# Performance work log

Measured on AMD Instinct MI355X. Metric: run time of the kernel, lower is better.

The kernel has to match this reference:

```python
import jax, jax.numpy as jnp
import numpy as np

EPS = 1e-7
N_NODES = 100000

# --- Lorentz model (c = 1), working at the origin o = (1, 0, ..., 0) ---

def expmap0(v_spatial):
    """Exp map at origin: tangent spatial part [N, d] -> hyperboloid point [N, d+1]."""
    nrm = jnp.sqrt(jnp.maximum(jnp.sum(v_spatial * v_spatial, axis=-1, keepdims=True), EPS))
    x0 = jnp.cosh(nrm)
    xs = jnp.sinh(nrm) / nrm * v_spatial
    return jnp.concatenate([x0, xs], axis=-1)


def logmap0(x):
    """Log map at origin: point [N, d+1] -> tangent spatial part [N, d]."""
    x0 = jnp.maximum(x[..., :1], 1.0 + EPS)
    xs = x[..., 1:]
    nrm = jnp.sqrt(jnp.maximum(jnp.sum(xs * xs, axis=-1, keepdims=True), EPS))
    return jnp.arccosh(x0) / nrm * xs


def sigmoid_nonlin(x):
    # log map -> sigmoid in tangent space -> exp map (c_in = c_out = 1)
    return expmap0(jax.nn.sigmoid(logmap0(x)))


def hgcn_layer(x, edge_index, W, b):
    """HGCN conv: tangent-space linear + mean aggregation over edges + exp map."""
    t = logmap0(x)                      # [N, d_in]
    h = t @ W + b                       # [N, d_out]
    src, dst = edge_index[0], edge_index[1]
    msg = h[src]                        # [E, d_out] gather
    agg = jax.ops.segment_sum(msg, dst, num_segments=N_NODES)
    deg = jax.ops.segment_sum(jnp.ones((edge_index.shape[1],), h.dtype), dst,
                              num_segments=N_NODES)
    agg = agg / jnp.maximum(deg, 1.0)[:, None]
    return expmap0(agg)


def setup_inputs() -> dict:
    key = jax.random.key(0)
    ks = jax.random.split(key, 10)
    d_in, h1, h2, h_mlp, d_out = 64, 64, 64, 128, 40
    return {
        "features": jax.random.normal(ks[0], (N_NODES, d_in), jnp.float32),
        "edge_index": jax.random.randint(ks[1], (2, 1600000), 0, N_NODES, jnp.int64),
        "W1": jax.random.normal(ks[2], (d_in, h1), jnp.float32) * 0.05,
        "b1": jnp.zeros((h1,), jnp.float32),
        "W2": jax.random.normal(ks[3], (h1, h2), jnp.float32) * 0.05,
        "b2": jnp.zeros((h2,), jnp.float32),
        "W3": jax.random.normal(ks[4], (h2, h_mlp), jnp.float32) * 0.05,
        "b3": jnp.zeros((h_mlp,), jnp.float32),
        "W4": jax.random.normal(ks[5], (h_mlp, d_out), jnp.float32) * 0.05,
        "b4": jnp.zeros((d_out,), jnp.float32),
    }


def reference(features, edge_index, W1, b1, W2, b2, W3, b3, W4, b4):
    # lift Euclidean features to the hyperboloid (pad time coord, exp map)
    x = expmap0(features)                       # [N, d_in+1]
    x = hgcn_layer(x, edge_index, W1, b1)
    x = sigmoid_nonlin(x)
    x = hgcn_layer(x, edge_index, W2, b2)
    x = sigmoid_nonlin(x)
    t = logmap0(x)                              # [N, h2] (spatial part, drops time coord)
    # MLP head (dropout inactive at eval)
    h = jax.nn.relu(t @ W3 + b3)
    return h @ W4 + b4
```

## Files before the change

kernel.cpp:

```cpp
#include <hip/hip_runtime.h>


constexpr int CSHIFT = 9;
constexpr int CNODES = 1 << CSHIFT;
constexpr int EPB    = 4096;
constexpr int EPT    = EPB / 256;
constexpr int CAP    = 16384;

constexpr int W1F_OFF = 0;
constexpr int W2F_OFF = 4096;
constexpr int W3F_OFF = 8192;
constexpr int W4F_OFF = 16384;
constexpr int WIMG_TOT = 22528;

typedef __attribute__((ext_vector_type(8))) short short8;
typedef __attribute__((ext_vector_type(4))) float floatx4;

__device__ __forceinline__ float sigmoidf(float x) {
    return 1.0f / (1.0f + __expf(-x));
}
__device__ __forceinline__ unsigned short f2bf(float f) {
    unsigned int u = __float_as_uint(f);
    u = (u + 0x7FFFu + ((u >> 16) & 1u)) >> 16;
    return (unsigned short)u;
}

__global__ __launch_bounds__(256) void prep_cast_k(
    const float* __restrict__ feat, unsigned short* __restrict__ featbf,
    const float* __restrict__ W1, const float* __restrict__ W2,
    const float* __restrict__ W3, const float* __restrict__ W4,
    unsigned short* __restrict__ img, int n8)
{
    int i = blockIdx.x * 256 + threadIdx.x;
    if (i < n8) {
        const float4* p = (const float4*)feat + (size_t)i * 2;
        float4 a = p[0], b = p[1];
        uint4 o;
        o.x = (unsigned)f2bf(a.x) | ((unsigned)f2bf(a.y) << 16);
        o.y = (unsigned)f2bf(a.z) | ((unsigned)f2bf(a.w) << 16);
        o.z = (unsigned)f2bf(b.x) | ((unsigned)f2bf(b.y) << 16);
        o.w = (unsigned)f2bf(b.z) | ((unsigned)f2bf(b.w) << 16);
        ((uint4*)featbf)[i] = o;
        return;
    }
    int t = i - n8;
    if (t >= WIMG_TOT) return;
    float v = 0.f;
    int s = t;
    if (s < W2F_OFF) {
        int j = s & 7, m = (s >> 3) & 15, q = (s >> 7) & 3, kk = (s >> 9) & 1, c = s >> 10;
        v = W1[(kk * 32 + q * 8 + j) * 64 + c * 16 + m];
    } else if (s < W3F_OFF) {
        s -= W2F_OFF;
        int j = s & 7, m = (s >> 3) & 15, q = (s >> 7) & 3, kk = (s >> 9) & 1, c = s >> 10;
        v = W2[(kk * 32 + q * 8 + j) * 64 + c * 16 + m];
    } else if (s < W4F_OFF) {
        s -= W3F_OFF;
        int j = s & 7, m = (s >> 3) & 15, q = (s >> 7) & 3, kk = (s >> 9) & 1, c = s >> 10;
        v = W3[(kk * 32 + q * 8 + j) * 128 + c * 16 + m];
    } else {
        s -= W4F_OFF;
        int j = s & 7, m = (s >> 3) & 15, q = (s >> 7) & 3, kk = (s >> 9) & 3, c = s >> 11;
        int n = c * 16 + m;
        if (n < 40) v = W4[(kk * 32 + q * 8 + j) * 40 + n];
    }
    img[t] = f2bf(v);
}

__global__ __launch_bounds__(256) void part_a(const int* __restrict__ src,
                                              const int* __restrict__ dst,
                                              int* __restrict__ ccur,
                                              int* __restrict__ arena,
                                              int E, int NBUCK) {
    __shared__ int  hist[256];
    __shared__ int  exoff[256];
    __shared__ int  lcur[256];
    __shared__ int  gbase[256];
    __shared__ int  stage[EPB];
    __shared__ unsigned char stageB[EPB];

    const int tid = threadIdx.x;
    const int e0  = blockIdx.x * EPB;
    const int ec  = min(EPB, E - e0);

    int pk[EPT], bk[EPT];
    hist[tid] = 0;
    __syncthreads();
    #pragma unroll
    for (int j = 0; j < EPT; j++) {
        int idx = tid + j * 256;
        if (idx < ec) {
            int s = src[e0 + idx];
            int d = dst[e0 + idx];
            bk[j] = d >> CSHIFT;
            pk[j] = s | ((d & (CNODES - 1)) << 17);
            atomicAdd(&hist[bk[j]], 1);
        } else bk[j] = -1;
    }
    __syncthreads();
    const int h = hist[tid];
    exoff[tid] = h;
    __syncthreads();
    for (int dd = 1; dd < 256; dd <<= 1) {
        int v = 0;
        if (tid >= dd) v = exoff[tid - dd];
        __syncthreads();
        if (tid >= dd) exoff[tid] += v;
        __syncthreads();
    }
    const int ex = exoff[tid] - h;
    int gb = 0;
    if (tid < NBUCK && h > 0) gb = atomicAdd(ccur + tid, h);
    __syncthreads();
    exoff[tid] = ex;
    lcur[tid]  = ex;
    gbase[tid] = gb;
    __syncthreads();
    #pragma unroll
    for (int j = 0; j < EPT; j++) {
        if (bk[j] >= 0) {
            int l = atomicAdd(&lcur[bk[j]], 1);
            stage[l]  = pk[j];
            stageB[l] = (unsigned char)bk[j];
        }
    }
    __syncthreads();
    for (int i = tid; i < ec; i += 256) {
        int b = stageB[i];
        arena[(size_t)b * CAP + gbase[b] + (i - exoff[b])] = stage[i];
    }
}

__global__ __launch_bounds__(256) void csr_fine(const int* __restrict__ arena,
                                                const int* __restrict__ ccur,
                                                int* __restrict__ off,
                                                int* __restrict__ ssrc,
                                                int N, int E, int NBUCK) {
    __shared__ int cnt[CNODES];
    __shared__ int cur[CNODES];
    __shared__ int part[256];
    const int b = blockIdx.x;
    const int node0 = b << CSHIFT;
    const int tid = threadIdx.x;

    part[tid] = (tid < NBUCK) ? ccur[tid] : 0;
    __syncthreads();
    for (int d = 1; d < 256; d <<= 1) {
        int v = 0;
        if (tid >= d) v = part[tid - d];
        __syncthreads();
        if (tid >= d) part[tid] += v;
        __syncthreads();
    }
    const int cbeg = (b > 0) ? part[b - 1] : 0;
    const int ec   = ccur[b];
    if (b == 0 && tid == 0) off[N] = E;
    __syncthreads();

    const int* pe = arena + (size_t)b * CAP;
    cnt[tid] = 0;
    cnt[tid + 256] = 0;
    __syncthreads();
    for (int i = tid; i < ec; i += 256)
        atomicAdd(&cnt[(pe[i] >> 17) & (CNODES - 1)], 1);
    __syncthreads();
    const int c0 = cnt[2 * tid], c1 = cnt[2 * tid + 1];
    part[tid] = c0 + c1;
    __syncthreads();
    for (int d = 1; d < 256; d <<= 1) {
        int v = 0;
        if (tid >= d) v = part[tid - d];
        __syncthreads();
        if (tid >= d) part[tid] += v;
        __syncthreads();
    }
    const int ex = (tid > 0) ? part[tid - 1] : 0;
    cur[2 * tid]     = ex;
    cur[2 * tid + 1] = ex + c0;
    if (node0 + 2 * tid     < N) off[node0 + 2 * tid]     = cbeg + ex;
    if (node0 + 2 * tid + 1 < N) off[node0 + 2 * tid + 1] = cbeg + ex + c0;
    __syncthreads();
    for (int i = tid; i < ec; i += 256) {
        int p = pe[i];
        int pos = cbeg + atomicAdd(&cur[(p >> 17) & (CNODES - 1)], 1);
        ssrc[pos] = p & 0x1FFFF;
    }
}

#define ACC8(v)                                    \
    acc[0] += __uint_as_float((v).x << 16);        \
    acc[1] += __uint_as_float((v).x & 0xFFFF0000u);\
    acc[2] += __uint_as_float((v).y << 16);        \
    acc[3] += __uint_as_float((v).y & 0xFFFF0000u);\
    acc[4] += __uint_as_float((v).z << 16);        \
    acc[5] += __uint_as_float((v).z & 0xFFFF0000u);\
    acc[6] += __uint_as_float((v).w << 16);        \
    acc[7] += __uint_as_float((v).w & 0xFFFF0000u);

__global__ __launch_bounds__(256) void agg_k(const unsigned short* __restrict__ h,
                                             const int* __restrict__ off,
                                             const int* __restrict__ ssrc,
                                             unsigned short* __restrict__ outb,
                                             int N) {
    int t = blockIdx.x * 256 + threadIdx.x;
    int g = t >> 3;
    if (g >= N) return;
    int q = (t & 7) * 8;
    int beg = off[g], end = off[g + 1];
    float acc[8] = {0.f, 0.f, 0.f, 0.f, 0.f, 0.f, 0.f, 0.f};
    int i = beg;
    for (; i + 8 <= end; i += 8) {
        uint4 v0 = *(const uint4*)(h + (size_t)ssrc[i]     * 64 + q);
        uint4 v1 = *(const uint4*)(h + (size_t)ssrc[i + 1] * 64 + q);
        uint4 v2 = *(const uint4*)(h + (size_t)ssrc[i + 2] * 64 + q);
        uint4 v3 = *(const uint4*)(h + (size_t)ssrc[i + 3] * 64 + q);
        uint4 v4 = *(const uint4*)(h + (size_t)ssrc[i + 4] * 64 + q);
        uint4 v5 = *(const uint4*)(h + (size_t)ssrc[i + 5] * 64 + q);
        uint4 v6 = *(const uint4*)(h + (size_t)ssrc[i + 6] * 64 + q);
        uint4 v7 = *(const uint4*)(h + (size_t)ssrc[i + 7] * 64 + q);
        ACC8(v0); ACC8(v1); ACC8(v2); ACC8(v3);
        ACC8(v4); ACC8(v5); ACC8(v6); ACC8(v7);
    }
    for (; i + 2 <= end; i += 2) {
        uint4 v0 = *(const uint4*)(h + (size_t)ssrc[i]     * 64 + q);
        uint4 v1 = *(const uint4*)(h + (size_t)ssrc[i + 1] * 64 + q);
        ACC8(v0); ACC8(v1);
    }
    for (; i < end; i++) {
        uint4 v = *(const uint4*)(h + (size_t)ssrc[i] * 64 + q);
        ACC8(v);
    }
    float inv = 1.0f / (float)max(end - beg, 1);
    uint4 p;
    p.x = (unsigned)f2bf(acc[0] * inv) | ((unsigned)f2bf(acc[1] * inv) << 16);
    p.y = (unsigned)f2bf(acc[2] * inv) | ((unsigned)f2bf(acc[3] * inv) << 16);
    p.z = (unsigned)f2bf(acc[4] * inv) | ((unsigned)f2bf(acc[5] * inv) << 16);
    p.w = (unsigned)f2bf(acc[6] * inv) | ((unsigned)f2bf(acc[7] * inv) << 16);
    *(uint4*)(outb + (size_t)g * 64 + q) = p;
}

__global__ __launch_bounds__(256) void gemmsig_k(
    const unsigned short* __restrict__ Abf, const int* __restrict__ off,
    const unsigned short* __restrict__ img, const float* __restrict__ bias,
    unsigned short* __restrict__ out, int N)
{
    const int tid = threadIdx.x;
    const int rowB = blockIdx.x * 64;
    const int w = tid >> 6, lane = tid & 63;
    const int m = lane & 15, quad = lane >> 4;
    const int row0 = rowB + w * 16;
    const int arow = min(row0 + m, N - 1);
    const short8* Wf = (const short8*)(img + W1F_OFF);

    floatx4 acc[4];
    #pragma unroll
    for (int c = 0; c < 4; c++) acc[c] = (floatx4){0.f, 0.f, 0.f, 0.f};
    #pragma unroll
    for (int kk = 0; kk < 2; kk++) {
        short8 a = *(const short8*)(Abf + (size_t)arow * 64 + kk * 32 + quad * 8);
        #pragma unroll
        for (int c = 0; c < 4; c++) {
            short8 b = Wf[((c * 2 + kk) * 4 + quad) * 16 + m];
            acc[c] = __builtin_amdgcn_mfma_f32_16x16x32_bf16(a, b, acc[c], 0, 0, 0);
        }
    }
    bool dzr[4];
    int rows[4];
    #pragma unroll
    for (int r = 0; r < 4; r++) {
        rows[r] = row0 + quad * 4 + r;
        dzr[r] = (rows[r] < N) ? (off[rows[r] + 1] == off[rows[r]]) : false;
    }
    #pragma unroll
    for (int c = 0; c < 4; c++) {
        int col = c * 16 + m;
        float bv = bias[col];
        #pragma unroll
        for (int r = 0; r < 4; r++) {
            if (rows[r] < N) {
                float v = dzr[r] ? 0.5f : sigmoidf(acc[c][r] + bv);
                out[(size_t)rows[r] * 64 + col] = f2bf(v);
            }
        }
    }
}

__global__ __launch_bounds__(256) void ep3b_k(
    const unsigned short* __restrict__ Abf, const int* __restrict__ off,
    const unsigned short* __restrict__ img,
    const float* __restrict__ b2, const float* __restrict__ b3,
    const float* __restrict__ b4, float* __restrict__ out, int N)
{
    __shared__ alignas(16) unsigned short T2[64 * 72];
    __shared__ alignas(16) unsigned short H3[64 * 136];

    const int tid = threadIdx.x;
    const int rowB = blockIdx.x * 64;
    const int w = tid >> 6, lane = tid & 63;
    const int m = lane & 15, quad = lane >> 4;
    const int row0 = rowB + w * 16;

    {
        const short8* Wf = (const short8*)(img + W2F_OFF);
        floatx4 acc[4];
        #pragma unroll
        for (int c = 0; c < 4; c++) acc[c] = (floatx4){0.f, 0.f, 0.f, 0.f};
        const int arow = min(row0 + m, N - 1);
        #pragma unroll
        for (int kk = 0; kk < 2; kk++) {
            short8 a = *(const short8*)(Abf + (size_t)arow * 64 + kk * 32 + quad * 8);
            #pragma unroll
            for (int c = 0; c < 4; c++) {
                short8 b = Wf[((c * 2 + kk) * 4 + quad) * 16 + m];
                acc[c] = __builtin_amdgcn_mfma_f32_16x16x32_bf16(a, b, acc[c], 0, 0, 0);
            }
        }
        bool dzr[4];
        #pragma unroll
        for (int r = 0; r < 4; r++) {
            int row = row0 + quad * 4 + r;
            dzr[r] = (row < N) ? (off[row + 1] == off[row]) : false;
        }
        #pragma unroll
        for (int c = 0; c < 4; c++) {
            int col = c * 16 + m;
            float bv = b2[col];
            #pragma unroll
            for (int r = 0; r < 4; r++) {
                int rl = w * 16 + quad * 4 + r;
                float v = dzr[r] ? 0.5f : sigmoidf(acc[c][r] + bv);
                T2[rl * 72 + col] = f2bf(v);
            }
        }
    }
    __syncthreads();

    {
        const short8* Wf = (const short8*)(img + W3F_OFF);
        floatx4 acc[8];
        #pragma unroll
        for (int c = 0; c < 8; c++) acc[c] = (floatx4){0.f, 0.f, 0.f, 0.f};
        #pragma unroll
        for (int kk = 0; kk < 2; kk++) {
            short8 a = *(const short8*)(T2 + (w * 16 + m) * 72 + kk * 32 + quad * 8);
            #pragma unroll
            for (int c = 0; c < 8; c++) {
                short8 b = Wf[((c * 2 + kk) * 4 + quad) * 16 + m];
                acc[c] = __builtin_amdgcn_mfma_f32_16x16x32_bf16(a, b, acc[c], 0, 0, 0);
            }
        }
        #pragma unroll
        for (int c = 0; c < 8; c++) {
            int col = c * 16 + m;
            float bv = b3[col];
            #pragma unroll
            for (int r = 0; r < 4; r++) {
                int rl = w * 16 + quad * 4 + r;
                H3[rl * 136 + col] = f2bf(fmaxf(acc[c][r] + bv, 0.f));
            }
        }
    }
    __syncthreads();

    {
        const short8* Wf = (const short8*)(img + W4F_OFF);
        floatx4 acc[3];
        #pragma unroll
        for (int c = 0; c < 3; c++) acc[c] = (floatx4){0.f, 0.f, 0.f, 0.f};
        #pragma unroll
        for (int kk = 0; kk < 4; kk++) {
            short8 a = *(const short8*)(H3 + (w * 16 + m) * 136 + kk * 32 + quad * 8);
            #pragma unroll
            for (int c = 0; c < 3; c++) {
                short8 b = Wf[((c * 4 + kk) * 4 + quad) * 16 + m];
                acc[c] = __builtin_amdgcn_mfma_f32_16x16x32_bf16(a, b, acc[c], 0, 0, 0);
            }
        }
        #pragma unroll
        for (int c = 0; c < 3; c++) {
            int col = c * 16 + m;
            if (col < 40) {
                float bv = b4[col];
                #pragma unroll
                for (int r = 0; r < 4; r++) {
                    int row = row0 + quad * 4 + r;
                    if (row < N) out[(size_t)row * 40 + col] = acc[c][r] + bv;
                }
            }
        }
    }
}

extern "C" void kernel_launch(void* const* d_in, const int* in_sizes, int n_in,
                              void* d_out, int out_size, void* d_ws, size_t ws_size,
                              hipStream_t stream)
{
    const float* feat = (const float*)d_in[0];
    const int*   eidx = (const int*)d_in[1];
    const float* W1 = (const float*)d_in[2];
    const float* b1 = (const float*)d_in[3];
    const float* W2 = (const float*)d_in[4];
    const float* b2 = (const float*)d_in[5];
    const float* W3 = (const float*)d_in[6];
    const float* b3 = (const float*)d_in[7];
    const float* W4 = (const float*)d_in[8];
    const float* b4 = (const float*)d_in[9];

    const int N = in_sizes[0] / 64;
    const int E = in_sizes[1] / 2;
    const int* src = eidx;
    const int* dst = eidx + E;

    const int NBUCK = (N + CNODES - 1) / CNODES;

    unsigned short* featbf = (unsigned short*)d_ws;
    unsigned short* t1     = featbf + (size_t)N * 64;
    unsigned short* aggF   = t1     + (size_t)N * 64;
    unsigned short* img    = aggF   + (size_t)N * 64;
    int*   off   = (int*)(img + WIMG_TOT);
    int*   ccur  = off + (N + 1);
    int*   ssrc  = ccur + NBUCK;
    int*   arena = ssrc + E;
    float* out   = (float*)d_out;

    hipMemsetAsync(ccur, 0, (size_t)NBUCK * sizeof(int), stream);

    const dim3 blk(256);
    const int gP  = (E + EPB - 1) / EPB;
    const int g64 = (N + 63) / 64;
    const int n8  = N * 64 / 8;
    const int gPC = (n8 + WIMG_TOT + 255) / 256;
    const int gAg = (int)(((size_t)N * 8 + 255) / 256);

    prep_cast_k<<<gPC, blk, 0, stream>>>(feat, featbf, W1, W2, W3, W4, img, n8);
    part_a<<<gP, blk, 0, stream>>>(src, dst, ccur, arena, E, NBUCK);
    csr_fine<<<NBUCK, blk, 0, stream>>>(arena, ccur, off, ssrc, N, E, NBUCK);

    agg_k<<<gAg, blk, 0, stream>>>(featbf, off, ssrc, aggF, N);
    gemmsig_k<<<g64, blk, 0, stream>>>(aggF, off, img, b1, t1, N);
    agg_k<<<gAg, blk, 0, stream>>>(t1, off, ssrc, aggF, N);
    ep3b_k<<<g64, blk, 0, stream>>>(aggF, off, img, b2, b3, b4, out, N);
}
```

Baseline: 235.9 us.

## Fuse neighbor aggregation into the following GEMM kernels via shared-memory tiles

Each 64-row block now gathers and mean-aggregates its rows' neighbor features into an LDS tile, then runs the MFMA GEMM straight from LDS. This removes two separate aggregation kernels and the global round trip of the aggregated buffer. In exchange, each thread handles two rows serially, so a block's gather has less parallelism and is exposed to degree imbalance. The second fused kernel shares LDS between the gather tile and H3 and adds a barrier to prevent overwriting.

```diff
diff --git a/kernel.cpp b/kernel.cpp
--- a/kernel.cpp
+++ b/kernel.cpp
@@ -197,59 +197,66 @@
     acc[6] += __uint_as_float((v).w << 16);        \
     acc[7] += __uint_as_float((v).w & 0xFFFF0000u);
 
-__global__ __launch_bounds__(256) void agg_k(const unsigned short* __restrict__ h,
-                                             const int* __restrict__ off,
-                                             const int* __restrict__ ssrc,
-                                             unsigned short* __restrict__ outb,
-                                             int N) {
-    int t = blockIdx.x * 256 + threadIdx.x;
-    int g = t >> 3;
-    if (g >= N) return;
-    int q = (t & 7) * 8;
-    int beg = off[g], end = off[g + 1];
-    float acc[8] = {0.f, 0.f, 0.f, 0.f, 0.f, 0.f, 0.f, 0.f};
-    int i = beg;
-    for (; i + 8 <= end; i += 8) {
-        uint4 v0 = *(const uint4*)(h + (size_t)ssrc[i]     * 64 + q);
-        uint4 v1 = *(const uint4*)(h + (size_t)ssrc[i + 1] * 64 + q);
-        uint4 v2 = *(const uint4*)(h + (size_t)ssrc[i + 2] * 64 + q);
-        uint4 v3 = *(const uint4*)(h + (size_t)ssrc[i + 3] * 64 + q);
-        uint4 v4 = *(const uint4*)(h + (size_t)ssrc[i + 4] * 64 + q);
-        uint4 v5 = *(const uint4*)(h + (size_t)ssrc[i + 5] * 64 + q);
-        uint4 v6 = *(const uint4*)(h + (size_t)ssrc[i + 6] * 64 + q);
-        uint4 v7 = *(const uint4*)(h + (size_t)ssrc[i + 7] * 64 + q);
-        ACC8(v0); ACC8(v1); ACC8(v2); ACC8(v3);
-        ACC8(v4); ACC8(v5); ACC8(v6); ACC8(v7);
-    }
-    for (; i + 2 <= end; i += 2) {
-        uint4 v0 = *(const uint4*)(h + (size_t)ssrc[i]     * 64 + q);
-        uint4 v1 = *(const uint4*)(h + (size_t)ssrc[i + 1] * 64 + q);
-        ACC8(v0); ACC8(v1);
-    }
-    for (; i < end; i++) {
-        uint4 v = *(const uint4*)(h + (size_t)ssrc[i] * 64 + q);
-        ACC8(v);
-    }
-    float inv = 1.0f / (float)max(end - beg, 1);
-    uint4 p;
-    p.x = (unsigned)f2bf(acc[0] * inv) | ((unsigned)f2bf(acc[1] * inv) << 16);
-    p.y = (unsigned)f2bf(acc[2] * inv) | ((unsigned)f2bf(acc[3] * inv) << 16);
-    p.z = (unsigned)f2bf(acc[4] * inv) | ((unsigned)f2bf(acc[5] * inv) << 16);
-    p.w = (unsigned)f2bf(acc[6] * inv) | ((unsigned)f2bf(acc[7] * inv) << 16);
-    *(uint4*)(outb + (size_t)g * 64 + q) = p;
-}
-
-__global__ __launch_bounds__(256) void gemmsig_k(
-    const unsigned short* __restrict__ Abf, const int* __restrict__ off,
-    const unsigned short* __restrict__ img, const float* __restrict__ bias,
-    unsigned short* __restrict__ out, int N)
+__device__ __forceinline__ void gather_tile(
+    const unsigned short* __restrict__ h, const int* __restrict__ off,
+    const int* __restrict__ ssrc, unsigned short* Agg, int rowB, int N, int tid)
 {
+    #pragma unroll
+    for (int pass = 0; pass < 2; pass++) {
+        int rl = pass * 32 + (tid >> 3);
+        int g  = rowB + rl;
+        int q  = (tid & 7) * 8;
+        uint4 p = make_uint4(0u, 0u, 0u, 0u);
+        if (g < N) {
+            int beg = off[g], end = off[g + 1];
+            float acc[8] = {0.f, 0.f, 0.f, 0.f, 0.f, 0.f, 0.f, 0.f};
+            int i = beg;
+            for (; i + 8 <= end; i += 8) {
+                uint4 v0 = *(const uint4*)(h + (size_t)ssrc[i]     * 64 + q);
+                uint4 v1 = *(const uint4*)(h + (size_t)ssrc[i + 1] * 64 + q);
+                uint4 v2 = *(const uint4*)(h + (size_t)ssrc[i + 2] * 64 + q);
+                uint4 v3 = *(const uint4*)(h + (size_t)ssrc[i + 3] * 64 + q);
+                uint4 v4 = *(const uint4*)(h + (size_t)ssrc[i + 4] * 64 + q);
+                uint4 v5 = *(const uint4*)(h + (size_t)ssrc[i + 5] * 64 + q);
+                uint4 v6 = *(const uint4*)(h + (size_t)ssrc[i + 6] * 64 + q);
+                uint4 v7 = *(const uint4*)(h + (size_t)ssrc[i + 7] * 64 + q);
+                ACC8(v0); ACC8(v1); ACC8(v2); ACC8(v3);
+                ACC8(v4); ACC8(v5); ACC8(v6); ACC8(v7);
+            }
+            for (; i + 2 <= end; i += 2) {
+                uint4 v0 = *(const uint4*)(h + (size_t)ssrc[i]     * 64 + q);
+                uint4 v1 = *(const uint4*)(h + (size_t)ssrc[i + 1] * 64 + q);
+                ACC8(v0); ACC8(v1);
+            }
+            for (; i < end; i++) {
+                uint4 v = *(const uint4*)(h + (size_t)ssrc[i] * 64 + q);
+                ACC8(v);
+            }
+            float inv = 1.0f / (float)max(end - beg, 1);
+            p.x = (unsigned)f2bf(acc[0]*inv) | ((unsigned)f2bf(acc[1]*inv) << 16);
+            p.y = (unsigned)f2bf(acc[2]*inv) | ((unsigned)f2bf(acc[3]*inv) << 16);
+            p.z = (unsigned)f2bf(acc[4]*inv) | ((unsigned)f2bf(acc[5]*inv) << 16);
+            p.w = (unsigned)f2bf(acc[6]*inv) | ((unsigned)f2bf(acc[7]*inv) << 16);
+        }
+        *(uint4*)(Agg + rl * 72 + q) = p;
+    }
+}
+
+__global__ __launch_bounds__(256) void aggemm1_k(
+    const unsigned short* __restrict__ featbf, const int* __restrict__ off,
+    const int* __restrict__ ssrc, const unsigned short* __restrict__ img,
+    const float* __restrict__ bias, unsigned short* __restrict__ t1, int N)
+{
+    __shared__ alignas(16) unsigned short Agg[64 * 72];
+
     const int tid = threadIdx.x;
     const int rowB = blockIdx.x * 64;
+    gather_tile(featbf, off, ssrc, Agg, rowB, N, tid);
+    __syncthreads();
+
     const int w = tid >> 6, lane = tid & 63;
     const int m = lane & 15, quad = lane >> 4;
     const int row0 = rowB + w * 16;
-    const int arow = min(row0 + m, N - 1);
     const short8* Wf = (const short8*)(img + W1F_OFF);
 
     floatx4 acc[4];
@@ -257,7 +264,7 @@
     for (int c = 0; c < 4; c++) acc[c] = (floatx4){0.f, 0.f, 0.f, 0.f};
     #pragma unroll
     for (int kk = 0; kk < 2; kk++) {
-        short8 a = *(const short8*)(Abf + (size_t)arow * 64 + kk * 32 + quad * 8);
+        short8 a = *(const short8*)(Agg + (w * 16 + m) * 72 + kk * 32 + quad * 8);
         #pragma unroll
         for (int c = 0; c < 4; c++) {
             short8 b = Wf[((c * 2 + kk) * 4 + quad) * 16 + m];
@@ -279,23 +286,28 @@
         for (int r = 0; r < 4; r++) {
             if (rows[r] < N) {
                 float v = dzr[r] ? 0.5f : sigmoidf(acc[c][r] + bv);
-                out[(size_t)rows[r] * 64 + col] = f2bf(v);
-            }
-        }
-    }
-}
-
-__global__ __launch_bounds__(256) void ep3b_k(
-    const unsigned short* __restrict__ Abf, const int* __restrict__ off,
-    const unsigned short* __restrict__ img,
+                t1[(size_t)rows[r] * 64 + col] = f2bf(v);
+            }
+        }
+    }
+}
+
+__global__ __launch_bounds__(256) void aggep3_k(
+    const unsigned short* __restrict__ t1, const int* __restrict__ off,
+    const int* __restrict__ ssrc, const unsigned short* __restrict__ img,
     const float* __restrict__ b2, const float* __restrict__ b3,
     const float* __restrict__ b4, float* __restrict__ out, int N)
 {
-    __shared__ alignas(16) unsigned short T2[64 * 72];
-    __shared__ alignas(16) unsigned short H3[64 * 136];
+    __shared__ alignas(16) unsigned short SM[13312];
+    unsigned short* T2  = SM;
+    unsigned short* Agg = SM + 4608;
+    unsigned short* H3  = SM + 4608;
 
     const int tid = threadIdx.x;
     const int rowB = blockIdx.x * 64;
+    gather_tile(t1, off, ssrc, Agg, rowB, N, tid);
+    __syncthreads();
+
     const int w = tid >> 6, lane = tid & 63;
     const int m = lane & 15, quad = lane >> 4;
     const int row0 = rowB + w * 16;
@@ -305,10 +317,9 @@
         floatx4 acc[4];
         #pragma unroll
         for (int c = 0; c < 4; c++) acc[c] = (floatx4){0.f, 0.f, 0.f, 0.f};
-        const int arow = min(row0 + m, N - 1);
         #pragma unroll
         for (int kk = 0; kk < 2; kk++) {
-            short8 a = *(const short8*)(Abf + (size_t)arow * 64 + kk * 32 + quad * 8);
+            short8 a = *(const short8*)(Agg + (w * 16 + m) * 72 + kk * 32 + quad * 8);
             #pragma unroll
             for (int c = 0; c < 4; c++) {
                 short8 b = Wf[((c * 2 + kk) * 4 + quad) * 16 + m];
@@ -321,6 +332,7 @@
             int row = row0 + quad * 4 + r;
             dzr[r] = (row < N) ? (off[row + 1] == off[row]) : false;
         }
+        __syncthreads();
         #pragma unroll
         for (int c = 0; c < 4; c++) {
             int col = c * 16 + m;
@@ -415,8 +427,7 @@
 
     unsigned short* featbf = (unsigned short*)d_ws;
     unsigned short* t1     = featbf + (size_t)N * 64;
-    unsigned short* aggF   = t1     + (size_t)N * 64;
-    unsigned short* img    = aggF   + (size_t)N * 64;
+    unsigned short* img    = t1     + (size_t)N * 64;
     int*   off   = (int*)(img + WIMG_TOT);
     int*   ccur  = off + (N + 1);
     int*   ssrc  = ccur + NBUCK;
@@ -430,14 +441,11 @@
     const int g64 = (N + 63) / 64;
     const int n8  = N * 64 / 8;
     const int gPC = (n8 + WIMG_TOT + 255) / 256;
-    const int gAg = (int)(((size_t)N * 8 + 255) / 256);
 
     prep_cast_k<<<gPC, blk, 0, stream>>>(feat, featbf, W1, W2, W3, W4, img, n8);
     part_a<<<gP, blk, 0, stream>>>(src, dst, ccur, arena, E, NBUCK);
     csr_fine<<<NBUCK, blk, 0, stream>>>(arena, ccur, off, ssrc, N, E, NBUCK);
 
-    agg_k<<<gAg, blk, 0, stream>>>(featbf, off, ssrc, aggF, N);
-    gemmsig_k<<<g64, blk, 0, stream>>>(aggF, off, img, b1, t1, N);
-    agg_k<<<gAg, blk, 0, stream>>>(t1, off, ssrc, aggF, N);
-    ep3b_k<<<g64, blk, 0, stream>>>(aggF, off, img, b2, b3, b4, out, N);
-}
+    aggemm1_k<<<g64, blk, 0, stream>>>(featbf, off, ssrc, img, b1, t1, N);
+    aggep3_k<<<g64, blk, 0, stream>>>(t1, off, ssrc, img, b2, b3, b4, out, N);
+}
```

Measured after the change: 234.6 us. No clear change (-0.5%).
